# Performance work log

Hardware: AMD Instinct MI355X
Metric: run time of the kernel (lower is better)

## Reference

```python
import jax, jax.numpy as jnp
import numpy as np
from math import sqrt

SCALE = sqrt(512.0)  # max(key_size, attn_hidden_size, query_size) with scaled=True

def setup_inputs() -> dict:
    key = jax.random.key(0)
    k1, k2, k3, k4, k5 = jax.random.split(key, 5)
    B, T, S, M, N, H = 8, 512, 512, 512, 512, 128
    return {
        "query": jax.random.normal(k1, (B, T, M), dtype=jnp.float32),
        "keys": jax.random.normal(k2, (B, S, N), dtype=jnp.float32),
        "W1": jax.random.normal(k3, (N, H), dtype=jnp.float32),
        "W2": jax.random.normal(k4, (M, H), dtype=jnp.float32),
        "v": jax.random.normal(k5, (H,), dtype=jnp.float32),
    }

def reference(query, keys, W1, W2, v):
    # Project query and keys into attention hidden space
    x1 = jnp.einsum('btm,mh->bth', query, W2)   # (B,T,H)
    x2 = jnp.einsum('bsn,nh->bsh', keys, W1)    # (B,S,H)
    # Broadcast merge (op='add'), tanh activation, v-weighted reduction over H
    merged = jnp.tanh(x1[:, :, None, :] + x2[:, None, :, :])  # (B,T,S,H)
    score = jnp.einsum('btsh,h->bts', merged, v)
    return score / SCALE
```

## Files before the change

### kernel.cpp

```cpp
#include <hip/hip_runtime.h>
#include <hip/hip_fp16.h>


constexpr float SCALE_IN  = 2.8853900817779268f;
constexpr float INV_SCALE = 0.04419417382415922f;

__global__ __launch_bounds__(512) void proj_kernel(
    const float* __restrict__ q,  const float* __restrict__ w2,
    const float* __restrict__ ky, const float* __restrict__ w1,
    unsigned int* __restrict__ x1w, unsigned int* __restrict__ x2w) {
  __shared__ float As[32 * 64];
  __shared__ float Ws[64 * 128];

  int blk = blockIdx.x;
  const float* A; const float* W; unsigned int* O;
  if (blk < 128) { A = q;  W = w2; O = x1w; }
  else           { blk -= 128; A = ky; W = w1; O = x2w; }
  const int rbase = blk * 32;
  const int tid = threadIdx.x;

  const int rq = tid >> 5;
  const int hq = tid & 31;

  float acc[2][4];
#pragma unroll
  for (int r = 0; r < 2; ++r)
#pragma unroll
    for (int c = 0; c < 4; ++c) acc[r][c] = 0.0f;

  for (int kb = 0; kb < 512; kb += 64) {
    {
      const int arow = tid >> 4;
      const int kq4  = (tid & 15) * 4;
      *(float4*)(As + arow * 64 + kq4) =
          *(const float4*)(A + (size_t)(rbase + arow) * 512 + kb + kq4);
      const int wrow = tid >> 5;
      const int hq4  = (tid & 31) * 4;
#pragma unroll
      for (int p = 0; p < 4; ++p)
        *(float4*)(Ws + (wrow + 16 * p) * 128 + hq4) =
            *(const float4*)(W + (size_t)(kb + wrow + 16 * p) * 128 + hq4);
    }
    __syncthreads();
#pragma unroll 4
    for (int k4 = 0; k4 < 64; k4 += 4) {
      float a[2][4], w[4][4];
      *(float4*)a[0] = *(const float4*)(As + (2 * rq + 0) * 64 + k4);
      *(float4*)a[1] = *(const float4*)(As + (2 * rq + 1) * 64 + k4);
#pragma unroll
      for (int kk = 0; kk < 4; ++kk)
        *(float4*)w[kk] = *(const float4*)(Ws + (k4 + kk) * 128 + 4 * hq);
#pragma unroll
      for (int kk = 0; kk < 4; ++kk)
#pragma unroll
        for (int r = 0; r < 2; ++r)
#pragma unroll
          for (int c = 0; c < 4; ++c)
            acc[r][c] = fmaf(a[r][kk], w[kk][c], acc[r][c]);
    }
    __syncthreads();
  }

#pragma unroll
  for (int r = 0; r < 2; ++r) {
    unsigned int pk[4];
#pragma unroll
    for (int c = 0; c < 4; ++c) {
      const float z  = acc[r][c] * SCALE_IN;
      const float kf = rintf(z);
      int ki = (int)kf;
      ki = max(min(ki, 511), -512);
      const float em = __builtin_amdgcn_exp2f(z - kf);
      pk[c] = (__float_as_uint(em) & 0xFFFFFC00u) | ((unsigned int)ki & 1023u);
    }
    *(uint4*)(O + (size_t)(rbase + 2 * rq + r) * 128 + 4 * hq) = *(uint4*)pk;
  }
}

__global__ __launch_bounds__(512, 4) void score_kernel(
    const unsigned int* __restrict__ x1w, const unsigned int* __restrict__ x2w,
    const float* __restrict__ v, float* __restrict__ out) {
  __shared__ unsigned int x1l[64 * 64];
  __shared__ unsigned int x2l[64 * 64];

  const int tid   = threadIdx.x;
  const int b     = blockIdx.x >> 6;
  const int tile  = blockIdx.x & 63;
  const int tbase = (tile >> 3) * 64;
  const int sbase = (tile & 7) * 64;

  const unsigned int* x1g = x1w + (size_t)(b * 512 + tbase) * 128;
  const unsigned int* x2g = x2w + (size_t)(b * 512 + sbase) * 128;

  const int sg = tid & 15;
  const int tg = tid >> 4;

  float racc[2][4];
#pragma unroll
  for (int i = 0; i < 2; ++i)
#pragma unroll
    for (int j = 0; j < 4; ++j) racc[i][j] = 0.0f;
  float sv = 0.0f;

  for (int ph = 0; ph < 2; ++ph) {
    {
      const int r1 = tid & 63;
      const int c0 = tid >> 6;
#pragma unroll
      for (int p = 0; p < 2; ++p) {
        const int c = c0 + 8 * p;
        const uint4 a =
            *(const uint4*)(x1g + (size_t)r1 * 128 + ph * 64 + 4 * c);
        x1l[(4 * c + 0) * 64 + r1] = a.x;
        x1l[(4 * c + 1) * 64 + r1] = a.y;
        x1l[(4 * c + 2) * 64 + r1] = a.z;
        x1l[(4 * c + 3) * 64 + r1] = a.w;
        const uint4 s =
            *(const uint4*)(x2g + (size_t)r1 * 128 + ph * 64 + 4 * c);
        x2l[(4 * c + 0) * 64 + r1] = s.x;
        x2l[(4 * c + 1) * 64 + r1] = s.y;
        x2l[(4 * c + 2) * 64 + r1] = s.z;
        x2l[(4 * c + 3) * 64 + r1] = s.w;
      }
    }
    __syncthreads();

    for (int hg = 0; hg < 16; ++hg) {
      const int h0 = hg * 4;
      const float4 vq = *(const float4*)(v + ph * 64 + h0);
      sv += (vq.x + vq.y) + (vq.z + vq.w);

      float emt[2][4]; int kt[2][4];
      float ems[4][4]; int ks[4][4];
#pragma unroll
      for (int qq = 0; qq < 4; ++qq) {
        const uint2 tp = *(const uint2*)(x1l + (h0 + qq) * 64 + 2 * tg);
        emt[0][qq] = __uint_as_float(tp.x);
        kt [0][qq] = (int)(tp.x << 22) >> 22;
        emt[1][qq] = __uint_as_float(tp.y);
        kt [1][qq] = (int)(tp.y << 22) >> 22;
        const uint4 sp = *(const uint4*)(x2l + (h0 + qq) * 64 + 4 * sg);
        ems[0][qq] = __uint_as_float(sp.x);
        ks [0][qq] = (int)(sp.x << 22) >> 22;
        ems[1][qq] = __uint_as_float(sp.y);
        ks [1][qq] = (int)(sp.y << 22) >> 22;
        ems[2][qq] = __uint_as_float(sp.z);
        ks [2][qq] = (int)(sp.z << 22) >> 22;
        ems[3][qq] = __uint_as_float(sp.w);
        ks [3][qq] = (int)(sp.w << 22) >> 22;
      }

#pragma unroll
      for (int i = 0; i < 2; ++i) {
#pragma unroll
        for (int j = 0; j < 4; ++j) {
          float e[4];
#pragma unroll
          for (int qq = 0; qq < 4; ++qq) {
            int kk = kt[i][qq] + ks[j][qq];
            kk = min(kk, 30);
            e[qq] = ldexpf(emt[i][qq] * ems[j][qq], kk);
          }
          const float a0 = e[0] + 1.0f, a1 = e[1] + 1.0f;
          const float a2 = e[2] + 1.0f, a3 = e[3] + 1.0f;
          const float p12 = a0 * a1, p34 = a2 * a3;
          float u1 = vq.x * a1; u1 = fmaf(vq.y, a0, u1);
          float u2 = vq.z * a3; u2 = fmaf(vq.w, a2, u2);
          float num = u1 * p34; num = fmaf(u2, p12, num);
          const float den = p12 * p34;
          racc[i][j] = fmaf(num, __builtin_amdgcn_rcpf(den), racc[i][j]);
        }
      }
    }
    __syncthreads();
  }

  const float c1v = sv * INV_SCALE;
  const float c2v = -2.0f * INV_SCALE;
#pragma unroll
  for (int i = 0; i < 2; ++i) {
    const int t = tbase + 2 * tg + i;
    float4 o;
    o.x = fmaf(racc[i][0], c2v, c1v);
    o.y = fmaf(racc[i][1], c2v, c1v);
    o.z = fmaf(racc[i][2], c2v, c1v);
    o.w = fmaf(racc[i][3], c2v, c1v);
    *(float4*)(out + (size_t)(b * 512 + t) * 512 + sbase + 4 * sg) = o;
  }
}

extern "C" void kernel_launch(void* const* d_in, const int* in_sizes, int n_in,
                              void* d_out, int out_size, void* d_ws, size_t ws_size,
                              hipStream_t stream) {
  const float* query = (const float*)d_in[0];
  const float* keys  = (const float*)d_in[1];
  const float* W1    = (const float*)d_in[2];
  const float* W2    = (const float*)d_in[3];
  const float* v     = (const float*)d_in[4];
  float* out = (float*)d_out;

  unsigned int* x1w = (unsigned int*)d_ws;
  unsigned int* x2w = x1w + 8 * 512 * 128;

  hipLaunchKernelGGL(proj_kernel, dim3(256), dim3(512), 0, stream,
                     query, W2, keys, W1, x1w, x2w);
  hipLaunchKernelGGL(score_kernel, dim3(512), dim3(512), 0, stream,
                     x1w, x2w, v, out);
}
```

Measured before the change: 146.1 us.

## Replace packed mantissa/exponent encoding with direct exp2 and split score into halves

```diff
diff --git a/kernel.cpp b/kernel.cpp
--- a/kernel.cpp
+++ b/kernel.cpp
@@ -8,14 +8,14 @@
 __global__ __launch_bounds__(512) void proj_kernel(
     const float* __restrict__ q,  const float* __restrict__ w2,
     const float* __restrict__ ky, const float* __restrict__ w1,
-    unsigned int* __restrict__ x1w, unsigned int* __restrict__ x2w) {
+    float* __restrict__ x1z, float* __restrict__ x2z) {
   __shared__ float As[32 * 64];
   __shared__ float Ws[64 * 128];
 
   int blk = blockIdx.x;
-  const float* A; const float* W; unsigned int* O;
-  if (blk < 128) { A = q;  W = w2; O = x1w; }
-  else           { blk -= 128; A = ky; W = w1; O = x2w; }
+  const float* A; const float* W; float* O;
+  if (blk < 128) { A = q;  W = w2; O = x1z; }
+  else           { blk -= 128; A = ky; W = w1; O = x2z; }
   const int rbase = blk * 32;
   const int tid = threadIdx.x;
 
@@ -63,43 +63,34 @@
 
 #pragma unroll
   for (int r = 0; r < 2; ++r) {
-    unsigned int pk[4];
-#pragma unroll
-    for (int c = 0; c < 4; ++c) {
-      const float z  = acc[r][c] * SCALE_IN;
-      const float kf = rintf(z);
-      int ki = (int)kf;
-      ki = max(min(ki, 511), -512);
-      const float em = __builtin_amdgcn_exp2f(z - kf);
-      pk[c] = (__float_as_uint(em) & 0xFFFFFC00u) | ((unsigned int)ki & 1023u);
-    }
-    *(uint4*)(O + (size_t)(rbase + 2 * rq + r) * 128 + 4 * hq) = *(uint4*)pk;
+    float4 z;
+    z.x = acc[r][0] * SCALE_IN;
+    z.y = acc[r][1] * SCALE_IN;
+    z.z = acc[r][2] * SCALE_IN;
+    z.w = acc[r][3] * SCALE_IN;
+    *(float4*)(O + (size_t)(rbase + 2 * rq + r) * 128 + 4 * hq) = z;
   }
 }
 
-__global__ __launch_bounds__(512, 4) void score_kernel(
-    const unsigned int* __restrict__ x1w, const unsigned int* __restrict__ x2w,
-    const float* __restrict__ v, float* __restrict__ out) {
-  __shared__ unsigned int x1l[64 * 64];
-  __shared__ unsigned int x2l[64 * 64];
+__global__ __launch_bounds__(512) void score_half_kernel(
+    const float* __restrict__ x1z, const float* __restrict__ x2z,
+    const float* __restrict__ v, float* __restrict__ out, int shalf) {
+  __shared__ float x1l[64 * 64];
+  __shared__ float x2l[64 * 32];
 
   const int tid   = threadIdx.x;
   const int b     = blockIdx.x >> 6;
   const int tile  = blockIdx.x & 63;
   const int tbase = (tile >> 3) * 64;
-  const int sbase = (tile & 7) * 64;
+  const int sbase = shalf * 256 + (tile & 7) * 32;
 
-  const unsigned int* x1g = x1w + (size_t)(b * 512 + tbase) * 128;
-  const unsigned int* x2g = x2w + (size_t)(b * 512 + sbase) * 128;
+  const float* x1g = x1z + (size_t)(b * 512 + tbase) * 128;
+  const float* x2g = x2z + (size_t)(b * 512 + sbase) * 128;
 
   const int sg = tid & 15;
   const int tg = tid >> 4;
 
-  float racc[2][4];
-#pragma unroll
-  for (int i = 0; i < 2; ++i)
-#pragma unroll
-    for (int j = 0; j < 4; ++j) racc[i][j] = 0.0f;
+  float racc[2][2] = {{0.0f, 0.0f}, {0.0f, 0.0f}};
   float sv = 0.0f;
 
   for (int ph = 0; ph < 2; ++ph) {
@@ -109,19 +100,21 @@
 #pragma unroll
       for (int p = 0; p < 2; ++p) {
         const int c = c0 + 8 * p;
-        const uint4 a =
-            *(const uint4*)(x1g + (size_t)r1 * 128 + ph * 64 + 4 * c);
+        const float4 a =
+            *(const float4*)(x1g + (size_t)r1 * 128 + ph * 64 + 4 * c);
         x1l[(4 * c + 0) * 64 + r1] = a.x;
         x1l[(4 * c + 1) * 64 + r1] = a.y;
         x1l[(4 * c + 2) * 64 + r1] = a.z;
         x1l[(4 * c + 3) * 64 + r1] = a.w;
-        const uint4 s =
-            *(const uint4*)(x2g + (size_t)r1 * 128 + ph * 64 + 4 * c);
-        x2l[(4 * c + 0) * 64 + r1] = s.x;
-        x2l[(4 * c + 1) * 64 + r1] = s.y;
-        x2l[(4 * c + 2) * 64 + r1] = s.z;
-        x2l[(4 * c + 3) * 64 + r1] = s.w;
       }
+      const int r2 = tid & 31;
+      const int c2 = tid >> 5;
+      const float4 s =
+          *(const float4*)(x2g + (size_t)r2 * 128 + ph * 64 + 4 * c2);
+      x2l[(4 * c2 + 0) * 32 + r2] = s.x;
+      x2l[(4 * c2 + 1) * 32 + r2] = s.y;
+      x2l[(4 * c2 + 2) * 32 + r2] = s.z;
+      x2l[(4 * c2 + 3) * 32 + r2] = s.w;
     }
     __syncthreads();
 
@@ -130,36 +123,27 @@
       const float4 vq = *(const float4*)(v + ph * 64 + h0);
       sv += (vq.x + vq.y) + (vq.z + vq.w);
 
-      float emt[2][4]; int kt[2][4];
-      float ems[4][4]; int ks[4][4];
+      float zt[2][4];
+      float zs[2][4];
 #pragma unroll
       for (int qq = 0; qq < 4; ++qq) {
-        const uint2 tp = *(const uint2*)(x1l + (h0 + qq) * 64 + 2 * tg);
-        emt[0][qq] = __uint_as_float(tp.x);
-        kt [0][qq] = (int)(tp.x << 22) >> 22;
-        emt[1][qq] = __uint_as_float(tp.y);
-        kt [1][qq] = (int)(tp.y << 22) >> 22;
-        const uint4 sp = *(const uint4*)(x2l + (h0 + qq) * 64 + 4 * sg);
-        ems[0][qq] = __uint_as_float(sp.x);
-        ks [0][qq] = (int)(sp.x << 22) >> 22;
-        ems[1][qq] = __uint_as_float(sp.y);
-        ks [1][qq] = (int)(sp.y << 22) >> 22;
-        ems[2][qq] = __uint_as_float(sp.z);
-        ks [2][qq] = (int)(sp.z << 22) >> 22;
-        ems[3][qq] = __uint_as_float(sp.w);
-        ks [3][qq] = (int)(sp.w << 22) >> 22;
+        const float2 tp = *(const float2*)(x1l + (h0 + qq) * 64 + 2 * tg);
+        zt[0][qq] = tp.x;
+        zt[1][qq] = tp.y;
+        const float2 sp = *(const float2*)(x2l + (h0 + qq) * 32 + 2 * sg);
+        zs[0][qq] = sp.x;
+        zs[1][qq] = sp.y;
       }
 
 #pragma unroll
       for (int i = 0; i < 2; ++i) {
 #pragma unroll
-        for (int j = 0; j < 4; ++j) {
+        for (int j = 0; j < 2; ++j) {
           float e[4];
 #pragma unroll
           for (int qq = 0; qq < 4; ++qq) {
-            int kk = kt[i][qq] + ks[j][qq];
-            kk = min(kk, 30);
-            e[qq] = ldexpf(emt[i][qq] * ems[j][qq], kk);
+            const float z = fminf(zt[i][qq] + zs[j][qq], 30.0f);
+            e[qq] = __builtin_amdgcn_exp2f(z);
           }
           const float a0 = e[0] + 1.0f, a1 = e[1] + 1.0f;
           const float a2 = e[2] + 1.0f, a3 = e[3] + 1.0f;
@@ -180,12 +164,10 @@
 #pragma unroll
   for (int i = 0; i < 2; ++i) {
     const int t = tbase + 2 * tg + i;
-    float4 o;
+    float2 o;
     o.x = fmaf(racc[i][0], c2v, c1v);
     o.y = fmaf(racc[i][1], c2v, c1v);
-    o.z = fmaf(racc[i][2], c2v, c1v);
-    o.w = fmaf(racc[i][3], c2v, c1v);
-    *(float4*)(out + (size_t)(b * 512 + t) * 512 + sbase + 4 * sg) = o;
+    *(float2*)(out + (size_t)(b * 512 + t) * 512 + sbase + 2 * sg) = o;
   }
 }
 
@@ -199,11 +181,13 @@
   const float* v     = (const float*)d_in[4];
   float* out = (float*)d_out;
 
-  unsigned int* x1w = (unsigned int*)d_ws;
-  unsigned int* x2w = x1w + 8 * 512 * 128;
+  float* x1zp = (float*)d_ws;
+  float* x2zp = x1zp + 8 * 512 * 128;
 
   hipLaunchKernelGGL(proj_kernel, dim3(256), dim3(512), 0, stream,
-                     query, W2, keys, W1, x1w, x2w);
-  hipLaunchKernelGGL(score_kernel, dim3(512), dim3(512), 0, stream,
-                     x1w, x2w, v, out);
+                     query, W2, keys, W1, x1zp, x2zp);
+  hipLaunchKernelGGL(score_half_kernel, dim3(512), dim3(512), 0, stream,
+                     x1zp, x2zp, v, out, 0);
+  hipLaunchKernelGGL(score_half_kernel, dim3(512), dim3(512), 0, stream,
+                     x1zp, x2zp, v, out, 1);
 }
```

New measurement: 147.0 us. Within noise of the previous version (+0.6%).
